# Performance work log

Hardware: AMD Instinct MI355X
Metric: run time of the kernel (lower is better)

The kernel has to match this reference:

```python
import jax, jax.numpy as jnp
import numpy as np

N, DIN, DOUT = 8192, 128, 128
NEG = -9.0e15  # the module's -9000000000000000.0 mask value
ALPHA = 0.2    # LeakyReLU negative slope


def setup_inputs() -> dict:
    key = jax.random.key(0)
    kx, ka, kw, ks, kr = jax.random.split(key, 5)
    X = jax.random.normal(kx, (N, DIN), dtype=jnp.float32)
    A = (jax.random.uniform(ka, (N, N)) < 0.01).astype(jnp.float32)
    A = A.at[jnp.arange(N), jnp.arange(N)].set(1.0)
    # Linear weight (Kaiming-uniform-ish range is irrelevant to math; use Xavier)
    lim_w = float(np.sqrt(6.0 / (DIN + DOUT)))
    W = jax.random.uniform(kw, (DOUT, DIN), jnp.float32, -lim_w, lim_w)
    b = jnp.zeros((DOUT,), jnp.float32)
    lim_a = float(np.sqrt(6.0 / (DOUT + 1)))
    a_s = jax.random.uniform(ks, (DOUT, 1), jnp.float32, -lim_a, lim_a)
    a_r = jax.random.uniform(kr, (DOUT, 1), jnp.float32, -lim_a, lim_a)
    return {"X": X, "A": A, "W": W, "b": b, "a_s": a_s, "a_r": a_r}


def reference(X, A, W, b, a_s, a_r):
    # H_in = Linear(X)
    H = X @ W.T + b                         # [N, DOUT]
    s = H @ a_s                             # [N, 1] source scores
    r = H @ a_r                             # [N, 1] receiver scores
    # M_s = A * s (broadcast over cols), M_r = A * r^T (broadcast over rows)
    e = jax.nn.leaky_relu(A * s + A * r.T, negative_slope=ALPHA)  # [N, N]
    masked = jnp.where(A > 0, e, NEG)
    att = jax.nn.softmax(masked, axis=1)    # row-stochastic attention
    H_out = att @ H                         # [N, DOUT]  (act = Identity, dropout = eval)
    # NOTE: the torch module applies LayerNorm into a local var but returns
    # the pre-norm H_out, so LayerNorm is dead code. A and [] passthroughs omitted.
    return H_out
```

## Files before the change

kernel.cpp:

```cpp
#include <hip/hip_runtime.h>

#define N 8192
#define D 128
#define ALPHA 0.2f
#define RCAP 256

typedef float fx4 __attribute__((ext_vector_type(4)));

__global__ __launch_bounds__(256) void linear_kernel(
    const float* __restrict__ X, const float* __restrict__ W,
    const float* __restrict__ b, const float* __restrict__ a_s,
    const float* __restrict__ a_r,
    float* __restrict__ H, float* __restrict__ sv, float* __restrict__ rv)
{
    __shared__ float Xs[128 * 36];
    __shared__ float Ws[64 * 132];

    const int tid = threadIdx.x;
    const int i0  = blockIdx.x * 32;

    for (int idx = tid; idx < 32 * 128; idx += 256) {
        const int row = idx >> 7, k = idx & 127;
        Xs[k * 36 + row] = X[(i0 + row) * D + k];
    }

    float acc[4][4] = {};
    const int ty = tid >> 5, tx = tid & 31;
    const int rbase = ty * 4, cbase = tx * 4;

    for (int kb = 0; kb < 2; ++kb) {
        __syncthreads();
        for (int idx = tid; idx < 64 * 128; idx += 256) {
            const int o = idx >> 6, kk = idx & 63;
            Ws[kk * 132 + o] = W[o * D + kb * 64 + kk];
        }
        __syncthreads();
        #pragma unroll
        for (int kk = 0; kk < 64; ++kk) {
            const float4 xv = *(const float4*)&Xs[(kb * 64 + kk) * 36 + rbase];
            const float4 wv = *(const float4*)&Ws[kk * 132 + cbase];
            const float xr[4] = {xv.x, xv.y, xv.z, xv.w};
            const float wc[4] = {wv.x, wv.y, wv.z, wv.w};
            #pragma unroll
            for (int r = 0; r < 4; ++r)
                #pragma unroll
                for (int c = 0; c < 4; ++c)
                    acc[r][c] += xr[r] * wc[c];
        }
    }

    const float4 bv  = *(const float4*)&b[cbase];
    const float4 asv = *(const float4*)&a_s[cbase];
    const float4 arv = *(const float4*)&a_r[cbase];
    #pragma unroll
    for (int r = 0; r < 4; ++r) {
        float4 h;
        h.x = acc[r][0] + bv.x;
        h.y = acc[r][1] + bv.y;
        h.z = acc[r][2] + bv.z;
        h.w = acc[r][3] + bv.w;
        *(float4*)&H[(size_t)(i0 + rbase + r) * D + cbase] = h;
        float ps = h.x * asv.x + h.y * asv.y + h.z * asv.z + h.w * asv.w;
        float pr = h.x * arv.x + h.y * arv.y + h.z * arv.z + h.w * arv.w;
        #pragma unroll
        for (int off = 16; off > 0; off >>= 1) {
            ps += __shfl_xor(ps, off);
            pr += __shfl_xor(pr, off);
        }
        if (tx == 0) {
            sv[i0 + rbase + r] = ps;
            rv[i0 + rbase + r] = pr;
        }
    }
}

__global__ __launch_bounds__(256) void attn_fused(
    const float* __restrict__ A, const float* __restrict__ H,
    const float* __restrict__ sv, const float* __restrict__ rv,
    float* __restrict__ out)
{
    __shared__ float2 s_l[RCAP];
    __shared__ int    s_wcnt[4];
    __shared__ float  s_red[8];
    __shared__ float4 s_part[4][32];

    const int tid  = threadIdx.x;
    const int wave = tid >> 6;
    const int lane = tid & 63;
    const int i    = blockIdx.x;

    const fx4* __restrict__ Arow = (const fx4*)(A + (size_t)i * N);

    unsigned m = 0;
    #pragma unroll
    for (int q = 0; q < 8; ++q) {
        const fx4 a = __builtin_nontemporal_load(&Arow[wave * 512 + q * 64 + lane]);
        m |= (a.x != 0.0f ? 1u : 0u) << (q * 4 + 0);
        m |= (a.y != 0.0f ? 1u : 0u) << (q * 4 + 1);
        m |= (a.z != 0.0f ? 1u : 0u) << (q * 4 + 2);
        m |= (a.w != 0.0f ? 1u : 0u) << (q * 4 + 3);
    }

    const int c = __popc(m);
    int scan = c;
    #pragma unroll
    for (int off = 1; off < 64; off <<= 1) {
        const int t = __shfl_up(scan, off);
        if (lane >= off) scan += t;
    }
    if (lane == 63) s_wcnt[wave] = scan;
    __syncthreads();
    int base = scan - c;
    #pragma unroll
    for (int w2 = 0; w2 < 4; ++w2)
        if (w2 < wave) base += s_wcnt[w2];
    int cnt = s_wcnt[0] + s_wcnt[1] + s_wcnt[2] + s_wcnt[3];
    cnt = (cnt < RCAP) ? cnt : RCAP;

    {
        unsigned mm = m;
        while (mm) {
            const int p = __ffs(mm) - 1;
            mm &= mm - 1;
            const int col = wave * 2048 + ((p >> 2) << 8) + (lane << 2) + (p & 3);
            if (base < RCAP) s_l[base].y = __int_as_float(col);
            ++base;
        }
    }
    __syncthreads();

    const float si = sv[i];
    float z = -3.0e38f;
    if (tid < cnt) {
        const int j = __float_as_int(s_l[tid].y);
        z = si + rv[j];
        z = (z > 0.0f) ? z : ALPHA * z;
    }
    float lm = z;
    #pragma unroll
    for (int off = 32; off > 0; off >>= 1) lm = fmaxf(lm, __shfl_xor(lm, off));
    if (lane == 0) s_red[wave] = lm;
    __syncthreads();
    const float M = fmaxf(fmaxf(s_red[0], s_red[1]), fmaxf(s_red[2], s_red[3]));

    const float w = (tid < cnt) ? __expf(z - M) : 0.0f;
    float sl = w;
    #pragma unroll
    for (int off = 32; off > 0; off >>= 1) sl += __shfl_xor(sl, off);
    if (lane == 0) s_red[4 + wave] = sl;
    __syncthreads();
    const float inv = 1.0f / (s_red[4] + s_red[5] + s_red[6] + s_red[7]);
    if (tid < cnt) s_l[tid].x = w * inv;
    __syncthreads();

    const int hw = tid >> 5;
    const int fs = tid & 31;
    float4 acc = make_float4(0.0f, 0.0f, 0.0f, 0.0f);
    #pragma unroll 4
    for (int p = hw; p < cnt; p += 8) {
        const float2 wj = s_l[p];
        const int   j  = __float_as_int(wj.y);
        const float4 h = *(const float4*)&H[(size_t)j * D + fs * 4];
        acc.x += wj.x * h.x;
        acc.y += wj.x * h.y;
        acc.z += wj.x * h.z;
        acc.w += wj.x * h.w;
    }
    acc.x += __shfl_xor(acc.x, 32);
    acc.y += __shfl_xor(acc.y, 32);
    acc.z += __shfl_xor(acc.z, 32);
    acc.w += __shfl_xor(acc.w, 32);
    if ((lane >> 5) == 0) s_part[wave][fs] = acc;
    __syncthreads();
    if (tid < 32) {
        float4 v = s_part[0][tid];
        const float4 v1 = s_part[1][tid];
        const float4 v2 = s_part[2][tid];
        const float4 v3 = s_part[3][tid];
        v.x += v1.x + v2.x + v3.x;
        v.y += v1.y + v2.y + v3.y;
        v.z += v1.z + v2.z + v3.z;
        v.w += v1.w + v2.w + v3.w;
        *(float4*)&out[(size_t)i * D + tid * 4] = v;
    }
}

extern "C" void kernel_launch(void* const* d_in, const int* in_sizes, int n_in,
                              void* d_out, int out_size, void* d_ws, size_t ws_size,
                              hipStream_t stream) {
    const float* X   = (const float*)d_in[0];
    const float* A   = (const float*)d_in[1];
    const float* W   = (const float*)d_in[2];
    const float* b   = (const float*)d_in[3];
    const float* a_s = (const float*)d_in[4];
    const float* a_r = (const float*)d_in[5];
    float* out = (float*)d_out;

    float* H  = (float*)d_ws;
    float* sv = H + (size_t)N * D;
    float* rv = sv + N;

    linear_kernel<<<256, 256, 0, stream>>>(X, W, b, a_s, a_r, H, sv, rv);
    attn_fused<<<N, 256, 0, stream>>>(A, H, sv, rv, out);
}
```

Baseline: 372.7 us.

## Assign one adjacency row per wavefront instead of per block

The attention kernel now has each 64-lane wave handle a whole row: it streams the 8192-column A row in 4 batches of 8 nontemporal loads, builds 64-bit masks, and compacts the neighbour list with wave-local scans. Every __syncthreads and shared-memory cross-wave reduction is replaced by wave barriers and shuffles, and the grid shrinks to N/4 blocks. This removes block-wide synchronisation and exposes more loads in flight per lane. The trade-off is less parallelism per row in the H gather phase (2 rows per step instead of 8) and higher register use per lane.

```diff
diff --git a/kernel.cpp b/kernel.cpp
--- a/kernel.cpp
+++ b/kernel.cpp
@@ -79,88 +79,102 @@
     const float* __restrict__ sv, const float* __restrict__ rv,
     float* __restrict__ out)
 {
-    __shared__ float2 s_l[RCAP];
-    __shared__ int    s_wcnt[4];
-    __shared__ float  s_red[8];
-    __shared__ float4 s_part[4][32];
+    __shared__ float2 s_l[4][RCAP];
 
     const int tid  = threadIdx.x;
     const int wave = tid >> 6;
     const int lane = tid & 63;
-    const int i    = blockIdx.x;
-
+    const int i    = (blockIdx.x << 2) + wave;
+
+    float2* __restrict__ sl = s_l[wave];
     const fx4* __restrict__ Arow = (const fx4*)(A + (size_t)i * N);
-
-    unsigned m = 0;
-    #pragma unroll
-    for (int q = 0; q < 8; ++q) {
-        const fx4 a = __builtin_nontemporal_load(&Arow[wave * 512 + q * 64 + lane]);
-        m |= (a.x != 0.0f ? 1u : 0u) << (q * 4 + 0);
-        m |= (a.y != 0.0f ? 1u : 0u) << (q * 4 + 1);
-        m |= (a.z != 0.0f ? 1u : 0u) << (q * 4 + 2);
-        m |= (a.w != 0.0f ? 1u : 0u) << (q * 4 + 3);
-    }
-
-    const int c = __popc(m);
+    const float si = sv[i];
+
+    unsigned long long m0 = 0ull, m1 = 0ull;
+    #pragma unroll
+    for (int g = 0; g < 4; ++g) {
+        fx4 a[8];
+        #pragma unroll
+        for (int q = 0; q < 8; ++q)
+            a[q] = __builtin_nontemporal_load(&Arow[(g * 8 + q) * 64 + lane]);
+        #pragma unroll
+        for (int q = 0; q < 8; ++q) {
+            const int kk = g * 8 + q;
+            unsigned long long bits =
+                (a[q].x != 0.0f ? 1ull : 0ull) |
+                (a[q].y != 0.0f ? 2ull : 0ull) |
+                (a[q].z != 0.0f ? 4ull : 0ull) |
+                (a[q].w != 0.0f ? 8ull : 0ull);
+            if (kk < 16) m0 |= bits << (kk * 4);
+            else         m1 |= bits << ((kk - 16) * 4);
+        }
+    }
+
+    const int c = __popcll(m0) + __popcll(m1);
     int scan = c;
     #pragma unroll
     for (int off = 1; off < 64; off <<= 1) {
         const int t = __shfl_up(scan, off);
         if (lane >= off) scan += t;
     }
-    if (lane == 63) s_wcnt[wave] = scan;
-    __syncthreads();
-    int base = scan - c;
-    #pragma unroll
-    for (int w2 = 0; w2 < 4; ++w2)
-        if (w2 < wave) base += s_wcnt[w2];
-    int cnt = s_wcnt[0] + s_wcnt[1] + s_wcnt[2] + s_wcnt[3];
+    int cnt = __shfl(scan, 63);
     cnt = (cnt < RCAP) ? cnt : RCAP;
-
-    {
-        unsigned mm = m;
-        while (mm) {
-            const int p = __ffs(mm) - 1;
-            mm &= mm - 1;
-            const int col = wave * 2048 + ((p >> 2) << 8) + (lane << 2) + (p & 3);
-            if (base < RCAP) s_l[base].y = __int_as_float(col);
-            ++base;
-        }
-    }
-    __syncthreads();
-
-    const float si = sv[i];
-    float z = -3.0e38f;
-    if (tid < cnt) {
-        const int j = __float_as_int(s_l[tid].y);
-        z = si + rv[j];
-        z = (z > 0.0f) ? z : ALPHA * z;
-    }
-    float lm = z;
+    int b = scan - c;
+
+    while (m0) {
+        const int p = (int)__ffsll(m0) - 1;
+        m0 &= m0 - 1;
+        const int col = ((p >> 2) << 8) + (lane << 2) + (p & 3);
+        if (b < RCAP) sl[b].y = __int_as_float(col);
+        ++b;
+    }
+    while (m1) {
+        const int p = (int)__ffsll(m1) - 1;
+        m1 &= m1 - 1;
+        const int col = (((p >> 2) + 16) << 8) + (lane << 2) + (p & 3);
+        if (b < RCAP) sl[b].y = __int_as_float(col);
+        ++b;
+    }
+    __builtin_amdgcn_wave_barrier();
+
+    float z[4];
+    #pragma unroll
+    for (int t = 0; t < 4; ++t) {
+        const int e = lane + (t << 6);
+        if (e < cnt) {
+            const int j = __float_as_int(sl[e].y);
+            const float v = si + rv[j];
+            z[t] = (v > 0.0f) ? v : ALPHA * v;
+        } else z[t] = -3.0e38f;
+    }
+    float lm = fmaxf(fmaxf(z[0], z[1]), fmaxf(z[2], z[3]));
     #pragma unroll
     for (int off = 32; off > 0; off >>= 1) lm = fmaxf(lm, __shfl_xor(lm, off));
-    if (lane == 0) s_red[wave] = lm;
-    __syncthreads();
-    const float M = fmaxf(fmaxf(s_red[0], s_red[1]), fmaxf(s_red[2], s_red[3]));
-
-    const float w = (tid < cnt) ? __expf(z - M) : 0.0f;
-    float sl = w;
-    #pragma unroll
-    for (int off = 32; off > 0; off >>= 1) sl += __shfl_xor(sl, off);
-    if (lane == 0) s_red[4 + wave] = sl;
-    __syncthreads();
-    const float inv = 1.0f / (s_red[4] + s_red[5] + s_red[6] + s_red[7]);
-    if (tid < cnt) s_l[tid].x = w * inv;
-    __syncthreads();
-
-    const int hw = tid >> 5;
-    const int fs = tid & 31;
+    float w[4];
+    float sume = 0.0f;
+    #pragma unroll
+    for (int t = 0; t < 4; ++t) {
+        w[t] = (lane + (t << 6) < cnt) ? __expf(z[t] - lm) : 0.0f;
+        sume += w[t];
+    }
+    #pragma unroll
+    for (int off = 32; off > 0; off >>= 1) sume += __shfl_xor(sume, off);
+    const float inv = 1.0f / sume;
+    #pragma unroll
+    for (int t = 0; t < 4; ++t) {
+        const int e = lane + (t << 6);
+        if (e < cnt) sl[e].x = w[t] * inv;
+    }
+    __builtin_amdgcn_wave_barrier();
+
+    const int hw = lane >> 5;
+    const int fs = lane & 31;
     float4 acc = make_float4(0.0f, 0.0f, 0.0f, 0.0f);
     #pragma unroll 4
-    for (int p = hw; p < cnt; p += 8) {
-        const float2 wj = s_l[p];
+    for (int p = hw; p < cnt; p += 2) {
+        const float2 wj = sl[p];
         const int   j  = __float_as_int(wj.y);
-        const float4 h = *(const float4*)&H[(size_t)j * D + fs * 4];
+        const float4 h = *(const float4*)&H[(size_t)j * D + (fs << 2)];
         acc.x += wj.x * h.x;
         acc.y += wj.x * h.y;
         acc.z += wj.x * h.z;
@@ -170,19 +184,8 @@
     acc.y += __shfl_xor(acc.y, 32);
     acc.z += __shfl_xor(acc.z, 32);
     acc.w += __shfl_xor(acc.w, 32);
-    if ((lane >> 5) == 0) s_part[wave][fs] = acc;
-    __syncthreads();
-    if (tid < 32) {
-        float4 v = s_part[0][tid];
-        const float4 v1 = s_part[1][tid];
-        const float4 v2 = s_part[2][tid];
-        const float4 v3 = s_part[3][tid];
-        v.x += v1.x + v2.x + v3.x;
-        v.y += v1.y + v2.y + v3.y;
-        v.z += v1.z + v2.z + v3.z;
-        v.w += v1.w + v2.w + v3.w;
-        *(float4*)&out[(size_t)i * D + tid * 4] = v;
-    }
+    if (hw == 0)
+        *(float4*)&out[(size_t)i * D + (fs << 2)] = acc;
 }
 
 extern "C" void kernel_launch(void* const* d_in, const int* in_sizes, int n_in,
@@ -201,5 +204,5 @@
     float* rv = sv + N;
 
     linear_kernel<<<256, 256, 0, stream>>>(X, W, b, a_s, a_r, H, sv, rv);
-    attn_fused<<<N, 256, 0, stream>>>(A, H, sv, rv, out);
+    attn_fused<<<N / 4, 256, 0, stream>>>(A, H, sv, rv, out);
 }
```

Result: no change. 372.4 us (-0.1%).
